# Performance work log

Hardware: AMD Instinct MI355X
Metric: run time of the kernel (lower is better)

## Reference

```python
import jax, jax.numpy as jnp
import numpy as np

N = 10000
IN_F = 512
OUT_F = 64
ALPHA = 0.2
NEG_INF = -9e15


def setup_inputs() -> dict:
    key = jax.random.key(0)
    k1, k2, k3, k4, k5, k6 = jax.random.split(key, 6)
    x = jax.random.normal(k1, (N, IN_F), dtype=jnp.float32)
    adj = jax.random.randint(k2, (N, N), 0, 2).astype(jnp.float32)
    M = jax.random.uniform(k3, (N, N), dtype=jnp.float32)
    W = jax.random.normal(k4, (IN_F, OUT_F), dtype=jnp.float32) * (1.414 / np.sqrt(IN_F))
    a_self = jax.random.normal(k5, (OUT_F, 1), dtype=jnp.float32) * 0.1
    a_neighs = jax.random.normal(k6, (OUT_F, 1), dtype=jnp.float32) * 0.1
    return {"x": x, "adj": adj, "M": M, "W": W, "a_self": a_self, "a_neighs": a_neighs}


def reference(x, adj, M, W, a_self, a_neighs):
    # h: [N, out_features]
    h = x @ W
    attn_for_self = h @ a_self      # [N, 1]
    attn_for_neighs = h @ a_neighs  # [N, 1]
    # outer-sum broadcast -> [N, N]
    attn_dense = attn_for_self + attn_for_neighs.T
    attn_dense = attn_dense * M
    attn_dense = jax.nn.leaky_relu(attn_dense, negative_slope=ALPHA)
    scores = jnp.where(adj > 0, attn_dense, NEG_INF)
    attention = jax.nn.softmax(scores, axis=1)
    h_prime = attention @ h  # [N, out_features]
    return jax.nn.elu(h_prime)  # concat=True path
```

## Files before the change

### kernel.cpp

```cpp
#include <hip/hip_runtime.h>
#include <math.h>

#define Nn 10000
#define NPAD 10048
#define INF_ 512
#define OUTF 64
#define ALPHA 0.2f
#define LOG2E 1.4426950408889634f

#define TI 32
#define TJ 64
#define NTILES ((Nn + TJ - 1) / TJ)
#define YS 4
#define TPC ((NTILES + YS - 1) / YS)

typedef __attribute__((ext_vector_type(8))) short bfrag;
typedef __attribute__((ext_vector_type(4))) float facc;

#define WS_S    0
#define WS_T    (Nn)
#define WS_TMAX (2*Nn)
#define WS_DEN  (2*Nn + 16)
#define WS_HP   (WS_DEN + YS*Nn)
#define WS_HBT  (WS_HP + YS*Nn*OUTF)

__device__ __forceinline__ unsigned short f2bf(float f) {
    unsigned int u = __float_as_uint(f);
    u += 0x7fffu + ((u >> 16) & 1u);
    return (unsigned short)(u >> 16);
}
__device__ __forceinline__ unsigned int pk2(float a, float b) {
    return (unsigned int)f2bf(a) | ((unsigned int)f2bf(b) << 16);
}

__global__ __launch_bounds__(256) void hgemm_kernel(
    const float* __restrict__ x, const float* __restrict__ W,
    const float* __restrict__ a_self, const float* __restrict__ a_neighs,
    unsigned short* __restrict__ hbfT, float* __restrict__ s, float* __restrict__ t)
{
    const int col  = threadIdx.x & 63;
    const int wid  = threadIdx.x >> 6;
    const int row0 = blockIdx.x * 16 + wid * 4;
    const float* x0 = x + row0 * INF_;

    float acc0 = 0.f, acc1 = 0.f, acc2 = 0.f, acc3 = 0.f;
    #pragma unroll 4
    for (int k4 = 0; k4 < INF_ / 4; ++k4) {
        const int k = k4 << 2;
        const float w0 = W[(k    ) * OUTF + col];
        const float w1 = W[(k + 1) * OUTF + col];
        const float w2 = W[(k + 2) * OUTF + col];
        const float w3 = W[(k + 3) * OUTF + col];
        const float4 xa = *(const float4*)(x0 +          k);
        const float4 xb = *(const float4*)(x0 +   INF_ + k);
        const float4 xc = *(const float4*)(x0 + 2*INF_ + k);
        const float4 xd = *(const float4*)(x0 + 3*INF_ + k);
        acc0 = fmaf(xa.x,w0, fmaf(xa.y,w1, fmaf(xa.z,w2, fmaf(xa.w,w3, acc0))));
        acc1 = fmaf(xb.x,w0, fmaf(xb.y,w1, fmaf(xb.z,w2, fmaf(xb.w,w3, acc1))));
        acc2 = fmaf(xc.x,w0, fmaf(xc.y,w1, fmaf(xc.z,w2, fmaf(xc.w,w3, acc2))));
        acc3 = fmaf(xd.x,w0, fmaf(xd.y,w1, fmaf(xd.z,w2, fmaf(xd.w,w3, acc3))));
    }
    ushort4 hb;
    hb.x = f2bf(acc0); hb.y = f2bf(acc1); hb.z = f2bf(acc2); hb.w = f2bf(acc3);
    *(ushort4*)(hbfT + (size_t)col * NPAD + row0) = hb;

    const float as = a_self[col], an = a_neighs[col];
    #define RED(ACC, U) { \
        float vs = (ACC) * as, vn = (ACC) * an; \
        _Pragma("unroll") \
        for (int d_ = 32; d_; d_ >>= 1) { vs += __shfl_xor(vs, d_); vn += __shfl_xor(vn, d_); } \
        if (col == 0) { s[row0 + (U)] = vs; t[row0 + (U)] = vn; } }
    RED(acc0, 0) RED(acc1, 1) RED(acc2, 2) RED(acc3, 3)
    #undef RED
}

__global__ __launch_bounds__(1024) void tmax_kernel(
    const float* __restrict__ t, float* __restrict__ tmax)
{
    __shared__ float red[16];
    float m = -3e38f;
    for (int i = threadIdx.x; i < Nn; i += 1024) m = fmaxf(m, t[i]);
    #pragma unroll
    for (int d = 32; d; d >>= 1) m = fmaxf(m, __shfl_xor(m, d));
    if ((threadIdx.x & 63) == 0) red[threadIdx.x >> 6] = m;
    __syncthreads();
    if (threadIdx.x < 16) {
        m = red[threadIdx.x];
        #pragma unroll
        for (int d = 8; d; d >>= 1) m = fmaxf(m, __shfl_xor(m, d));
        if (threadIdx.x == 0) *tmax = m;
    }
}

__global__ __launch_bounds__(256, 4) void gat_main_kernel(
    const float* __restrict__ adj, const float* __restrict__ Mm,
    const unsigned short* __restrict__ hbfT, const float* __restrict__ sv,
    const float* __restrict__ tv, const float* __restrict__ tmaxp,
    float* __restrict__ den_part, float* __restrict__ hp_part)
{
    __shared__ __align__(16) unsigned short hTl[2][OUTF][TJ + 8];
    __shared__ __align__(16) unsigned short Pl[2][TI][TJ + 8];

    const int tid = threadIdx.x;
    const int i0  = blockIdx.x * TI;
    const int tlo = blockIdx.y * TPC;
    const int thi = min(NTILES, tlo + TPC);

    const int rr = tid >> 3, jc = tid & 7;
    const int prow = i0 + rr;
    const bool rowok = prow < Nn;
    const float si = rowok ? sv[prow] : 0.0f;
    const float mc = fmaxf(0.0f, si + *tmaxp) * LOG2E;
    const float* aRow = adj + (size_t)prow * Nn;
    const float* mRow = Mm  + (size_t)prow * Nn;

    const int hc_ = tid >> 2, hseg = tid & 3;
    const unsigned short* hsrc = hbfT + (size_t)hc_ * NPAD + hseg * 16;

    const int lane = tid & 63, wv = tid >> 6;
    const int l15 = lane & 15, kq = lane >> 4;
    const int rb = wv & 1, cbp = wv >> 1;

    facc accA = {0.f, 0.f, 0.f, 0.f}, accB = {0.f, 0.f, 0.f, 0.f};
    float denacc = 0.0f;

    const float4 z4 = make_float4(0.f, 0.f, 0.f, 0.f);
    float4 pa0 = z4, pa1 = z4, pm0 = z4, pm1 = z4, pt0 = z4, pt1 = z4;
    uint4 ph0 = make_uint4(0,0,0,0), ph1 = make_uint4(0,0,0,0);

    auto prefetch = [&](int tile) {
        const int j0 = tile * TJ;
        ph0 = *(const uint4*)(hsrc + j0);
        ph1 = *(const uint4*)(hsrc + j0 + 8);
        const int jl = j0 + (jc << 3);
        if (rowok && jl + 7 < Nn) {
            pa0 = *(const float4*)(aRow + jl); pa1 = *(const float4*)(aRow + jl + 4);
            pm0 = *(const float4*)(mRow + jl); pm1 = *(const float4*)(mRow + jl + 4);
            pt0 = *(const float4*)(tv   + jl); pt1 = *(const float4*)(tv   + jl + 4);
        } else {
            pa0 = pa1 = pm0 = pm1 = pt0 = pt1 = z4;
            if (rowok) {
                #define LD1(dst, base, off) if ((jl + (off)) < Nn) dst = (base)[jl + (off)]
                LD1(pa0.x, aRow, 0); LD1(pa0.y, aRow, 1); LD1(pa0.z, aRow, 2); LD1(pa0.w, aRow, 3);
                LD1(pa1.x, aRow, 4); LD1(pa1.y, aRow, 5); LD1(pa1.z, aRow, 6); LD1(pa1.w, aRow, 7);
                LD1(pm0.x, mRow, 0); LD1(pm0.y, mRow, 1); LD1(pm0.z, mRow, 2); LD1(pm0.w, mRow, 3);
                LD1(pm1.x, mRow, 4); LD1(pm1.y, mRow, 5); LD1(pm1.z, mRow, 6); LD1(pm1.w, mRow, 7);
                LD1(pt0.x, tv,   0); LD1(pt0.y, tv,   1); LD1(pt0.z, tv,   2); LD1(pt0.w, tv,   3);
                LD1(pt1.x, tv,   4); LD1(pt1.y, tv,   5); LD1(pt1.z, tv,   6); LD1(pt1.w, tv,   7);
                #undef LD1
            }
        }
    };

    #define PC(dst, av, mv, tvv) { \
        float e_ = (si + (tvv)) * (mv); \
        float l_ = fmaxf(e_, ALPHA * e_); \
        dst = ((av) > 0.0f) ? exp2f(fmaf(l_, LOG2E, -mc)) : 0.0f; }

    auto stage = [&](int b) {
        *(uint4*)&hTl[b][hc_][hseg * 16]     = ph0;
        *(uint4*)&hTl[b][hc_][hseg * 16 + 8] = ph1;
        float4 p40, p41;
        PC(p40.x, pa0.x, pm0.x, pt0.x); PC(p40.y, pa0.y, pm0.y, pt0.y);
        PC(p40.z, pa0.z, pm0.z, pt0.z); PC(p40.w, pa0.w, pm0.w, pt0.w);
        PC(p41.x, pa1.x, pm1.x, pt1.x); PC(p41.y, pa1.y, pm1.y, pt1.y);
        PC(p41.z, pa1.z, pm1.z, pt1.z); PC(p41.w, pa1.w, pm1.w, pt1.w);
        denacc += ((p40.x + p40.y) + (p40.z + p40.w)) + ((p41.x + p41.y) + (p41.z + p41.w));
        uint4 pw;
        pw.x = pk2(p40.x, p40.y); pw.y = pk2(p40.z, p40.w);
        pw.z = pk2(p41.x, p41.y); pw.w = pk2(p41.z, p41.w);
        *(uint4*)&Pl[b][rr][jc << 3] = pw;
    };

    prefetch(tlo);
    stage(0);
    if (tlo + 1 < thi) prefetch(tlo + 1);

    for (int tile = tlo; tile < thi; ++tile) {
        const int cur = (tile - tlo) & 1;
        __syncthreads();

        const unsigned short* aP  = &Pl[cur][rb * 16 + l15][kq * 8];
        const unsigned short* bP0 = &hTl[cur][cbp * 32 + l15][kq * 8];
        const unsigned short* bP1 = bP0 + 16 * (TJ + 8);
        #pragma unroll
        for (int k0 = 0; k0 < TJ; k0 += 32) {
            const bfrag af = *(const bfrag*)(aP  + k0);
            const bfrag b0 = *(const bfrag*)(bP0 + k0);
            const bfrag b1 = *(const bfrag*)(bP1 + k0);
            accA = __builtin_amdgcn_mfma_f32_16x16x32_bf16(af, b0, accA, 0, 0, 0);
            accB = __builtin_amdgcn_mfma_f32_16x16x32_bf16(af, b1, accB, 0, 0, 0);
        }

        if (tile + 1 < thi) {
            stage(cur ^ 1);
            if (tile + 2 < thi) prefetch(tile + 2);
        }
    }
    #undef PC

    float d = denacc;
    d += __shfl_xor(d, 1); d += __shfl_xor(d, 2); d += __shfl_xor(d, 4);
    if (rowok && jc == 0) den_part[blockIdx.y * Nn + prow] = d;

    float* hp = hp_part + (size_t)blockIdx.y * (Nn * OUTF);
    const int orow = i0 + rb * 16 + (kq << 2);
    const int oc   = cbp * 32 + l15;
    #pragma unroll
    for (int r = 0; r < 4; ++r) {
        if (orow + r < Nn) {
            hp[(orow + r) * OUTF + oc]      = accA[r];
            hp[(orow + r) * OUTF + oc + 16] = accB[r];
        }
    }
}

__global__ __launch_bounds__(256) void finalize_kernel(
    const float* __restrict__ dp, const float* __restrict__ hp,
    float* __restrict__ out)
{
    const int idx = blockIdx.x * 256 + threadIdx.x;
    const int S = Nn * OUTF;
    const float num = (hp[idx] + hp[S + idx]) + (hp[2*S + idx] + hp[3*S + idx]);
    const int row = idx >> 6;
    const float den = (dp[row] + dp[Nn + row]) + (dp[2*Nn + row] + dp[3*Nn + row]);
    const float v = num / den;
    out[idx] = (v > 0.0f) ? v : expm1f(v);
}

extern "C" void kernel_launch(void* const* d_in, const int* in_sizes, int n_in,
                              void* d_out, int out_size, void* d_ws, size_t ws_size,
                              hipStream_t stream) {
    const float* x        = (const float*)d_in[0];
    const float* adj      = (const float*)d_in[1];
    const float* Mm       = (const float*)d_in[2];
    const float* W        = (const float*)d_in[3];
    const float* a_self   = (const float*)d_in[4];
    const float* a_neighs = (const float*)d_in[5];

    float* out  = (float*)d_out;
    float* ws   = (float*)d_ws;
    float* s    = ws + WS_S;
    float* t    = ws + WS_T;
    float* tmax = ws + WS_TMAX;
    float* denp = ws + WS_DEN;
    float* hpp  = ws + WS_HP;
    unsigned short* hbfT = (unsigned short*)(ws + WS_HBT);

    hgemm_kernel<<<Nn / 16, 256, 0, stream>>>(x, W, a_self, a_neighs, hbfT, s, t);
    tmax_kernel<<<1, 1024, 0, stream>>>(t, tmax);
    gat_main_kernel<<<dim3((Nn + TI - 1) / TI, YS), 256, 0, stream>>>(
        adj, Mm, hbfT, s, t, tmax, denp, hpp);
    finalize_kernel<<<(Nn * OUTF) / 256, 256, 0, stream>>>(denp, hpp, out);
}
```

Baseline: 261.4 us.

## Single-buffer LDS tiles, widen split-K to 6 slices, raise occupancy to 6 blocks

Replaces the double-buffered LDS staging with a single buffer and two barriers per tile. The global prefetch of the next tile is issued before the MFMA loop, fenced by a scheduling barrier so the loads overlap the matrix math. The column split (YS) rises from 4 to 6 and launch bounds now target 6 blocks per CU, giving more parallel blocks and waves to hide the memory-bound adj/M streaming. The cost is an extra barrier per tile, less compute/staging overlap within a block, and more partial results for finalize to reduce and write.

```diff
diff --git a/kernel.cpp b/kernel.cpp
--- a/kernel.cpp
+++ b/kernel.cpp
@@ -11,7 +11,7 @@
 #define TI 32
 #define TJ 64
 #define NTILES ((Nn + TJ - 1) / TJ)
-#define YS 4
+#define YS 6
 #define TPC ((NTILES + YS - 1) / YS)
 
 typedef __attribute__((ext_vector_type(8))) short bfrag;
@@ -92,14 +92,14 @@
     }
 }
 
-__global__ __launch_bounds__(256, 4) void gat_main_kernel(
+__global__ __launch_bounds__(256, 6) void gat_main_kernel(
     const float* __restrict__ adj, const float* __restrict__ Mm,
     const unsigned short* __restrict__ hbfT, const float* __restrict__ sv,
     const float* __restrict__ tv, const float* __restrict__ tmaxp,
     float* __restrict__ den_part, float* __restrict__ hp_part)
 {
-    __shared__ __align__(16) unsigned short hTl[2][OUTF][TJ + 8];
-    __shared__ __align__(16) unsigned short Pl[2][TI][TJ + 8];
+    __shared__ __align__(16) unsigned short hTl[OUTF][TJ + 8];
+    __shared__ __align__(16) unsigned short Pl[TI][TJ + 8];
 
     const int tid = threadIdx.x;
     const int i0  = blockIdx.x * TI;
@@ -120,6 +120,9 @@
     const int lane = tid & 63, wv = tid >> 6;
     const int l15 = lane & 15, kq = lane >> 4;
     const int rb = wv & 1, cbp = wv >> 1;
+    const unsigned short* aP  = &Pl[rb * 16 + l15][kq * 8];
+    const unsigned short* bP0 = &hTl[cbp * 32 + l15][kq * 8];
+    const unsigned short* bP1 = bP0 + 16 * (TJ + 8);
 
     facc accA = {0.f, 0.f, 0.f, 0.f}, accB = {0.f, 0.f, 0.f, 0.f};
     float denacc = 0.0f;
@@ -157,32 +160,30 @@
         float l_ = fmaxf(e_, ALPHA * e_); \
         dst = ((av) > 0.0f) ? exp2f(fmaf(l_, LOG2E, -mc)) : 0.0f; }
 
-    auto stage = [&](int b) {
-        *(uint4*)&hTl[b][hc_][hseg * 16]     = ph0;
-        *(uint4*)&hTl[b][hc_][hseg * 16 + 8] = ph1;
+    prefetch(tlo);
+    for (int tile = tlo; tile < thi; ++tile) {
+        __syncthreads();
+
+        *(uint4*)&hTl[hc_][hseg * 16]     = ph0;
+        *(uint4*)&hTl[hc_][hseg * 16 + 8] = ph1;
+
         float4 p40, p41;
         PC(p40.x, pa0.x, pm0.x, pt0.x); PC(p40.y, pa0.y, pm0.y, pt0.y);
         PC(p40.z, pa0.z, pm0.z, pt0.z); PC(p40.w, pa0.w, pm0.w, pt0.w);
         PC(p41.x, pa1.x, pm1.x, pt1.x); PC(p41.y, pa1.y, pm1.y, pt1.y);
         PC(p41.z, pa1.z, pm1.z, pt1.z); PC(p41.w, pa1.w, pm1.w, pt1.w);
         denacc += ((p40.x + p40.y) + (p40.z + p40.w)) + ((p41.x + p41.y) + (p41.z + p41.w));
+
         uint4 pw;
         pw.x = pk2(p40.x, p40.y); pw.y = pk2(p40.z, p40.w);
         pw.z = pk2(p41.x, p41.y); pw.w = pk2(p41.z, p41.w);
-        *(uint4*)&Pl[b][rr][jc << 3] = pw;
-    };
-
-    prefetch(tlo);
-    stage(0);
-    if (tlo + 1 < thi) prefetch(tlo + 1);
-
-    for (int tile = tlo; tile < thi; ++tile) {
-        const int cur = (tile - tlo) & 1;
+        *(uint4*)&Pl[rr][jc << 3] = pw;
+
         __syncthreads();
 
-        const unsigned short* aP  = &Pl[cur][rb * 16 + l15][kq * 8];
-        const unsigned short* bP0 = &hTl[cur][cbp * 32 + l15][kq * 8];
-        const unsigned short* bP1 = bP0 + 16 * (TJ + 8);
+        if (tile + 1 < thi) prefetch(tile + 1);
+        __builtin_amdgcn_sched_barrier(0);
+
         #pragma unroll
         for (int k0 = 0; k0 < TJ; k0 += 32) {
             const bfrag af = *(const bfrag*)(aP  + k0);
@@ -190,11 +191,6 @@
             const bfrag b1 = *(const bfrag*)(bP1 + k0);
             accA = __builtin_amdgcn_mfma_f32_16x16x32_bf16(af, b0, accA, 0, 0, 0);
             accB = __builtin_amdgcn_mfma_f32_16x16x32_bf16(af, b1, accB, 0, 0, 0);
-        }
-
-        if (tile + 1 < thi) {
-            stage(cur ^ 1);
-            if (tile + 2 < thi) prefetch(tile + 2);
         }
     }
     #undef PC
@@ -221,9 +217,13 @@
 {
     const int idx = blockIdx.x * 256 + threadIdx.x;
     const int S = Nn * OUTF;
-    const float num = (hp[idx] + hp[S + idx]) + (hp[2*S + idx] + hp[3*S + idx]);
     const int row = idx >> 6;
-    const float den = (dp[row] + dp[Nn + row]) + (dp[2*Nn + row] + dp[3*Nn + row]);
+    float num = 0.0f, den = 0.0f;
+    #pragma unroll
+    for (int y = 0; y < YS; ++y) {
+        num += hp[(size_t)y * S + idx];
+        den += dp[y * Nn + row];
+    }
     const float v = num / den;
     out[idx] = (v > 0.0f) ? v : expm1f(v);
 }
```

Result: slower. 274.4 us (+5.0%).
